# Optimization experiments

Measured on AMD Instinct MI355X. Metric: run time of the kernel, lower is better.

The kernel has to match this reference:

```python
import jax, jax.numpy as jnp
import numpy as np

N_LOCATIONS = 8192


def setup_inputs() -> dict:
    key = jax.random.key(0)
    k1, k2, k3 = jax.random.split(key, 3)
    N = N_LOCATIONS
    # index tensor: values in [0, N)
    w = jax.random.randint(k1, (512, 64), 0, N, dtype=jnp.int64)
    # Linear params: W is [out_features, in_features] as in torch.nn.Linear
    W = jax.random.normal(k2, (N, N), dtype=jnp.float32) / np.float32(np.sqrt(N))
    b = jax.random.normal(k3, (N,), dtype=jnp.float32) * 0.01
    return {"w": w, "W": W, "b": b}


def reference(w, W, b):
    # torch: one_hot(w).float() @ W.T + b
    # one_hot(w) @ W.T selects, for each token index i, column i of W,
    # i.e. row i of W.T. Express as a gather (same math, no dense one-hot).
    # out shape: [512, 64, N]
    return jnp.take(W.T, w, axis=0) + b
```

## Files before the change

### kernel.cpp

```cpp
#include <hip/hip_runtime.h>
#include <hip/hip_bf16.h>


constexpr int N     = 8192;
constexpr int TILE  = 64;
constexpr int NBKT  = N / TILE;

__global__ void init_k(int* counts_and_cursors) {
    int t = threadIdx.x;
    if (t < 2 * NBKT) counts_and_cursors[t] = 0;
}

__global__ void count_k(const int* __restrict__ w, int* __restrict__ counts, int n) {
    int t = blockIdx.x * blockDim.x + threadIdx.x;
    if (t < n) atomicAdd(&counts[w[t] >> 6], 1);
}

__global__ void scan_k(const int* __restrict__ counts, int* __restrict__ offsets) {
    if (threadIdx.x == 0) {
        int acc = 0;
        for (int i = 0; i < NBKT; ++i) { offsets[i] = acc; acc += counts[i]; }
        offsets[NBKT] = acc;
    }
}

__global__ void scatter_k(const int* __restrict__ w, const int* __restrict__ offsets,
                          int* __restrict__ cursors, int* __restrict__ sorted, int n) {
    int t = blockIdx.x * blockDim.x + threadIdx.x;
    if (t < n) {
        int i   = w[t];
        int bkt = i >> 6;
        int pos = atomicAdd(&cursors[bkt], 1);
        sorted[offsets[bkt] + pos] = (t << 6) | (i & 63);
    }
}

__global__ __launch_bounds__(256) void gather_k(const float* __restrict__ W,
                                                const float* __restrict__ b,
                                                const int* __restrict__ offsets,
                                                const int* __restrict__ sorted,
                                                float* __restrict__ out) {
    __shared__ float tile[TILE][TILE + 1];

    const int ct = blockIdx.x;
    const int rt = blockIdx.y;
    const int i0 = ct * TILE;
    const int j0 = rt * TILE;
    const int tid = threadIdx.x;

    {
        const int jr = tid >> 4;
        const int c4 = (tid & 15) << 2;
        #pragma unroll
        for (int r = 0; r < TILE; r += 16) {
            const int j = r + jr;
            const float4 v = *reinterpret_cast<const float4*>(
                &W[(size_t)(j0 + j) * N + i0 + c4]);
            tile[j][c4 + 0] = v.x;
            tile[j][c4 + 1] = v.y;
            tile[j][c4 + 2] = v.z;
            tile[j][c4 + 3] = v.w;
        }
    }
    const int lane = tid & 63;
    const int wave = tid >> 6;
    const float bv = b[j0 + lane];
    __syncthreads();

    const int beg = offsets[ct];
    const int end = offsets[ct + 1];
    for (int k = beg + wave; k < end; k += 4) {
        const int v  = sorted[k];
        const int t  = v >> 6;
        const int ii = v & 63;
        out[(size_t)t * N + j0 + lane] = tile[lane][ii] + bv;
    }
}

extern "C" void kernel_launch(void* const* d_in, const int* in_sizes, int n_in,
                              void* d_out, int out_size, void* d_ws, size_t ws_size,
                              hipStream_t stream) {
    const int*   w  = (const int*)d_in[0];
    const float* Wm = (const float*)d_in[1];
    const float* b  = (const float*)d_in[2];
    float* out = (float*)d_out;
    const int n = in_sizes[0];

    int* counts  = (int*)d_ws;
    int* cursors = counts  + NBKT;
    int* offsets = cursors + NBKT;
    int* sorted  = offsets + NBKT + 1;

    init_k<<<1, 256, 0, stream>>>(counts);
    count_k<<<(n + 255) / 256, 256, 0, stream>>>(w, counts, n);
    scan_k<<<1, 64, 0, stream>>>(counts, offsets);
    scatter_k<<<(n + 255) / 256, 256, 0, stream>>>(w, offsets, cursors, sorted, n);

    dim3 grid(NBKT, N / TILE);
    gather_k<<<grid, 256, 0, stream>>>(Wm, b, offsets, sorted, out);
}
```

Measured before the change: 1.281 ms.

## Fuse bucket sort into one block and widen gather tiles with swizzled LDS

The four preprocessing kernels (init, count, scan, scatter) become a single 1024-thread block that counts, scans and scatters through shared-memory atomics, which removes three launches and the global atomics. The gather kernel now covers 256 output columns per block instead of 64. Each sorted index read therefore feeds four output segments, and the grid has a quarter as many blocks. The padded LDS tile is replaced by an XOR-swizzled layout written with float4 stores, and the next sorted index is prefetched. The cost is a serial single-block sort and 64KB of LDS per block, which limits occupancy.

```diff
diff --git a/kernel.cpp b/kernel.cpp
--- a/kernel.cpp
+++ b/kernel.cpp
@@ -1,37 +1,42 @@
 #include <hip/hip_runtime.h>
-#include <hip/hip_bf16.h>
 
 
-constexpr int N     = 8192;
-constexpr int TILE  = 64;
-constexpr int NBKT  = N / TILE;
+constexpr int N    = 8192;
+constexpr int TILE = 64;
+constexpr int TJ   = 256;
+constexpr int NBKT = N / TILE;
 
-__global__ void init_k(int* counts_and_cursors) {
-    int t = threadIdx.x;
-    if (t < 2 * NBKT) counts_and_cursors[t] = 0;
-}
-
-__global__ void count_k(const int* __restrict__ w, int* __restrict__ counts, int n) {
-    int t = blockIdx.x * blockDim.x + threadIdx.x;
-    if (t < n) atomicAdd(&counts[w[t] >> 6], 1);
-}
-
-__global__ void scan_k(const int* __restrict__ counts, int* __restrict__ offsets) {
-    if (threadIdx.x == 0) {
-        int acc = 0;
-        for (int i = 0; i < NBKT; ++i) { offsets[i] = acc; acc += counts[i]; }
-        offsets[NBKT] = acc;
+__global__ __launch_bounds__(1024) void sort_k(const int* __restrict__ w, int n,
+                                               int* __restrict__ offsets,
+                                               int* __restrict__ sorted) {
+    __shared__ int cnt[NBKT];
+    __shared__ int sc[NBKT];
+    __shared__ int cur[NBKT];
+    const int tid = threadIdx.x;
+    if (tid < NBKT) cnt[tid] = 0;
+    __syncthreads();
+    for (int t = tid; t < n; t += 1024) atomicAdd(&cnt[w[t] >> 6], 1);
+    __syncthreads();
+    if (tid < NBKT) sc[tid] = cnt[tid];
+    __syncthreads();
+    for (int d = 1; d < NBKT; d <<= 1) {
+        int v = 0;
+        if (tid < NBKT && tid >= d) v = sc[tid - d];
+        __syncthreads();
+        if (tid < NBKT) sc[tid] += v;
+        __syncthreads();
     }
-}
-
-__global__ void scatter_k(const int* __restrict__ w, const int* __restrict__ offsets,
-                          int* __restrict__ cursors, int* __restrict__ sorted, int n) {
-    int t = blockIdx.x * blockDim.x + threadIdx.x;
-    if (t < n) {
-        int i   = w[t];
-        int bkt = i >> 6;
-        int pos = atomicAdd(&cursors[bkt], 1);
-        sorted[offsets[bkt] + pos] = (t << 6) | (i & 63);
+    if (tid < NBKT) {
+        const int off = sc[tid] - cnt[tid];
+        cur[tid] = off;
+        offsets[tid] = off;
+        if (tid == NBKT - 1) offsets[NBKT] = sc[tid];
+    }
+    __syncthreads();
+    for (int t = tid; t < n; t += 1024) {
+        const int i   = w[t];
+        const int pos = atomicAdd(&cur[i >> 6], 1);
+        sorted[pos] = (t << 6) | (i & 63);
     }
 }
 
@@ -40,40 +45,62 @@
                                                 const int* __restrict__ offsets,
                                                 const int* __restrict__ sorted,
                                                 float* __restrict__ out) {
-    __shared__ float tile[TILE][TILE + 1];
+    __shared__ alignas(16) float tile[TJ * TILE];
 
-    const int ct = blockIdx.x;
-    const int rt = blockIdx.y;
-    const int i0 = ct * TILE;
-    const int j0 = rt * TILE;
+    const int ct  = blockIdx.x;
+    const int rt  = blockIdx.y;
+    const int i0  = ct * TILE;
+    const int j0  = rt * TJ;
     const int tid = threadIdx.x;
 
     {
         const int jr = tid >> 4;
         const int c4 = (tid & 15) << 2;
         #pragma unroll
-        for (int r = 0; r < TILE; r += 16) {
+        for (int r = 0; r < TJ; r += 16) {
             const int j = r + jr;
             const float4 v = *reinterpret_cast<const float4*>(
                 &W[(size_t)(j0 + j) * N + i0 + c4]);
-            tile[j][c4 + 0] = v.x;
-            tile[j][c4 + 1] = v.y;
-            tile[j][c4 + 2] = v.z;
-            tile[j][c4 + 3] = v.w;
+            const int x = j & 31;
+            const int p = x & 3;
+            const float in[4] = {v.x, v.y, v.z, v.w};
+            float4 sv;
+            float* svp = reinterpret_cast<float*>(&sv);
+            #pragma unroll
+            for (int o = 0; o < 4; ++o) svp[o] = in[o ^ p];
+            *reinterpret_cast<float4*>(&tile[(j << 6) + (c4 ^ (x & ~3))]) = sv;
         }
     }
     const int lane = tid & 63;
     const int wave = tid >> 6;
-    const float bv = b[j0 + lane];
+    const float bv0 = b[j0 +       lane];
+    const float bv1 = b[j0 +  64 + lane];
+    const float bv2 = b[j0 + 128 + lane];
+    const float bv3 = b[j0 + 192 + lane];
     __syncthreads();
 
-    const int beg = offsets[ct];
-    const int end = offsets[ct + 1];
-    for (int k = beg + wave; k < end; k += 4) {
-        const int v  = sorted[k];
-        const int t  = v >> 6;
-        const int ii = v & 63;
-        out[(size_t)t * N + j0 + lane] = tile[lane][ii] + bv;
+    const int beg   = offsets[ct];
+    const int end   = offsets[ct + 1];
+    const int lx    = lane & 31;
+    const int lbase = lane << 6;
+
+    int k = beg + wave;
+    int v = (k < end) ? sorted[k] : 0;
+    for (; k < end; k += 4) {
+        const int kn = k + 4;
+        const int vn = (kn < end) ? sorted[kn] : 0;
+        const int t   = v >> 6;
+        const int isw = (v & 63) ^ lx;
+        const float r0 = tile[lbase           + isw];
+        const float r1 = tile[lbase +  1*4096 + isw];
+        const float r2 = tile[lbase +  2*4096 + isw];
+        const float r3 = tile[lbase +  3*4096 + isw];
+        float* o = out + (size_t)t * N + j0 + lane;
+        o[0]   = r0 + bv0;
+        o[64]  = r1 + bv1;
+        o[128] = r2 + bv2;
+        o[192] = r3 + bv3;
+        v = vn;
     }
 }
 
@@ -86,16 +113,11 @@
     float* out = (float*)d_out;
     const int n = in_sizes[0];
 
-    int* counts  = (int*)d_ws;
-    int* cursors = counts  + NBKT;
-    int* offsets = cursors + NBKT;
+    int* offsets = (int*)d_ws;
     int* sorted  = offsets + NBKT + 1;
 
-    init_k<<<1, 256, 0, stream>>>(counts);
-    count_k<<<(n + 255) / 256, 256, 0, stream>>>(w, counts, n);
-    scan_k<<<1, 64, 0, stream>>>(counts, offsets);
-    scatter_k<<<(n + 255) / 256, 256, 0, stream>>>(w, offsets, cursors, sorted, n);
+    sort_k<<<1, 1024, 0, stream>>>(w, n, offsets, sorted);
 
-    dim3 grid(NBKT, N / TILE);
+    dim3 grid(NBKT, N / TJ);
     gather_k<<<grid, 256, 0, stream>>>(Wm, b, offsets, sorted, out);
 }
```

Result: faster. 1.255 ms (-2.0%).
